# Kernel tuning notes

Hardware: AMD Instinct MI355X
Metric: run time of the kernel (lower is better)

The kernel has to match this reference:

```python
import jax, jax.numpy as jnp
import numpy as np

B, S, D, DEPTH = 2, 2048, 1024, 4
NUM_LEAVES = 2 ** DEPTH          # 16
NUM_DEC = NUM_LEAVES - 1         # 15


def setup_inputs() -> dict:
    key = jax.random.key(0)
    k1, k2, k3, k4, k5 = jax.random.split(key, 5)
    scale = 1.0 / np.sqrt(D)
    return {
        "x": jax.random.normal(k1, (B, S, D), dtype=jnp.float32),
        "dec_w": jax.random.normal(k2, (NUM_DEC, D), dtype=jnp.float32) * scale,
        "dec_b": jax.random.normal(k3, (NUM_DEC,), dtype=jnp.float32) * scale,
        "leaf_w": jax.random.normal(k4, (NUM_LEAVES, D, D), dtype=jnp.float32) * scale,  # [leaf, out, in] (torch Linear layout)
        "leaf_b": jax.random.normal(k5, (NUM_LEAVES, D), dtype=jnp.float32) * scale,
    }


def reference(x, dec_w, dec_b, leaf_w, leaf_b):
    num_leaves = leaf_w.shape[0]
    num_dec = num_leaves - 1
    # All decision-node sigmoids in one batched GEMM: [B,S,num_dec]
    dec = jax.nn.sigmoid(jnp.einsum("bsd,nd->bsn", x, dec_w) + dec_b)
    # Faithful to the original: each tree slot is multiplied exactly once by its
    # direct parent's decision (left child: p, right child: 1-p).
    leaf_idx = np.arange(num_dec, 2 * num_leaves - 1)      # slots holding leaf probs
    parent = (leaf_idx - 1) // 2                           # [num_leaves]
    is_left = (leaf_idx % 2 == 1)                          # [num_leaves]
    dec_p = dec[..., parent]                               # [B,S,num_leaves]
    leaf_probs = jnp.where(jnp.asarray(is_left), dec_p, 1.0 - dec_p)
    # All leaf MLPs as one batched GEMM: [B,S,L,D]
    leaf_out = jnp.einsum("bsd,lod->bslo", x, leaf_w) + leaf_b
    # Probability-weighted sum over leaves -> [B,S,D]
    return jnp.einsum("bslo,bsl->bso", leaf_out, leaf_probs)
```

## Files before the change

kernel.cpp:

```cpp
#include <hip/hip_runtime.h>
#include <stdint.h>


#define M_TOK 4096
#define DDIM  1024
#define KFLAT 9216

typedef __bf16 bf16x8 __attribute__((ext_vector_type(8)));
typedef float  f32x4  __attribute__((ext_vector_type(4)));
typedef unsigned short u16x4 __attribute__((ext_vector_type(4)));
typedef unsigned short u16x8 __attribute__((ext_vector_type(8)));

#define GLB(p) ((const __attribute__((address_space(1))) void*)(p))
#define LDS(p) ((__attribute__((address_space(3))) void*)(p))

__device__ __forceinline__ unsigned short f2bf(float f) {
    union { float f; uint32_t u; } v; v.f = f;
    uint32_t u = v.u;
    return (unsigned short)((u + 0x7fffu + ((u >> 16) & 1u)) >> 16);
}

__global__ __launch_bounds__(256) void prep_dec_kernel(
    const float* __restrict__ x, const float* __restrict__ dec_w,
    const float* __restrict__ dec_b, const float* __restrict__ lw,
    const float* __restrict__ lb, unsigned short* __restrict__ wp,
    float* __restrict__ bw, unsigned short* __restrict__ xs,
    float* __restrict__ pmat)
{
    if (blockIdx.x < 1024) {
        int idx = blockIdx.x * 256 + threadIdx.x;
        int o  = idx >> 8;
        int k4 = (idx & 255) << 2;
        size_t src = (size_t)o * DDIM + k4;
        size_t dstb = (size_t)o * KFLAT + k4;
        float4 acc = make_float4(0.f, 0.f, 0.f, 0.f);
#pragma unroll
        for (int j = 0; j < 8; ++j) {
            const float4 a = *(const float4*)(lw + (size_t)(2*j)   * DDIM*DDIM + src);
            const float4 b = *(const float4*)(lw + (size_t)(2*j+1) * DDIM*DDIM + src);
            u16x4 d;
            d[0] = f2bf(a.x - b.x); d[1] = f2bf(a.y - b.y);
            d[2] = f2bf(a.z - b.z); d[3] = f2bf(a.w - b.w);
            *(u16x4*)(wp + dstb + (size_t)j * DDIM) = d;
            acc.x += b.x; acc.y += b.y; acc.z += b.z; acc.w += b.w;
        }
        u16x4 s;
        s[0] = f2bf(acc.x); s[1] = f2bf(acc.y); s[2] = f2bf(acc.z); s[3] = f2bf(acc.w);
        *(u16x4*)(wp + dstb + (size_t)8 * DDIM) = s;
        if ((idx & 255) == 0) {
            float sb = 0.f;
#pragma unroll
            for (int j = 0; j < 8; ++j) {
                float ba = lb[(2*j) * DDIM + o];
                float bb = lb[(2*j+1) * DDIM + o];
                bw[j * DDIM + o] = ba - bb;
                sb += bb;
            }
            bw[8 * DDIM + o] = sb;
        }
    } else {
        int m    = (blockIdx.x - 1024) * 4 + (threadIdx.x >> 6);
        int lane = threadIdx.x & 63;
        const float* xr = x + (size_t)m * DDIM + lane * 16;
        float xv[16];
        *(float4*)&xv[0]  = *(const float4*)(xr + 0);
        *(float4*)&xv[4]  = *(const float4*)(xr + 4);
        *(float4*)&xv[8]  = *(const float4*)(xr + 8);
        *(float4*)&xv[12] = *(const float4*)(xr + 12);
        float s[8];
#pragma unroll
        for (int j = 0; j < 8; ++j) {
            const float* wr = dec_w + (size_t)(7 + j) * DDIM + lane * 16;
            float a = 0.f;
#pragma unroll
            for (int i = 0; i < 16; i += 4) {
                float4 wv = *(const float4*)(wr + i);
                a = fmaf(xv[i], wv.x, fmaf(xv[i+1], wv.y, fmaf(xv[i+2], wv.z, fmaf(xv[i+3], wv.w, a))));
            }
            s[j] = a;
        }
#pragma unroll
        for (int j = 0; j < 8; ++j)
#pragma unroll
            for (int off = 32; off > 0; off >>= 1)
                s[j] += __shfl_xor(s[j], off);
        float p[8];
#pragma unroll
        for (int j = 0; j < 8; ++j)
            p[j] = 1.0f / (1.0f + expf(-(s[j] + dec_b[7 + j])));
        if (lane == 0) {
#pragma unroll
            for (int j = 0; j < 8; ++j)
                pmat[(size_t)m * 8 + j] = p[j];
        }
#pragma unroll
        for (int j = 0; j < 9; ++j) {
            float pj = (j < 8) ? p[j] : 1.0f;
            unsigned short* dst = xs + (size_t)m * KFLAT + j * DDIM + lane * 16;
#pragma unroll
            for (int c = 0; c < 2; ++c) {
                u16x8 o;
#pragma unroll
                for (int e = 0; e < 8; ++e) o[e] = f2bf(pj * xv[c * 8 + e]);
                *(u16x8*)(dst + c * 8) = o;
            }
        }
    }
}

__global__ __launch_bounds__(256, 4) void tree_gemm3(
    const unsigned short* __restrict__ xs,
    const unsigned short* __restrict__ wp,
    const float* __restrict__ bw,
    const float* __restrict__ pmat,
    float* __restrict__ out,
    float* __restrict__ parts,
    int KG)
{
    __shared__ __align__(16) unsigned short Asm[2][128 * 32];
    __shared__ __align__(16) unsigned short Bsm[2][128 * 32];

    const int tid  = threadIdx.x;
    const int lane = tid & 63;
    const int w    = tid >> 6;
    const int wm   = w >> 1, wn = w & 1;
    const int bx   = blockIdx.x;
    const int xcd  = bx & 7;
    const int ii   = bx >> 3;
    const int mt   = xcd * 4 + (ii >> 3);
    const int nt   = ii & 7;
    const int m0   = mt * 128, n0 = nt * 128;
    const int g    = blockIdx.y;
    const int k0   = g * KG;
    const int ra   = lane & 15;
    const int kb   = (lane >> 4) * 8;

    f32x4 acc[4][4] = {};

    auto stage = [&](int buf, int t) {
#pragma unroll
        for (int c = 0; c < 2; ++c) {
            int row = w * 32 + c * 16 + (lane >> 2);
            int ke  = k0 + t * 32 + (lane & 3) * 8;
            const unsigned short* ga = xs + (size_t)(m0 + row) * KFLAT + ke;
            __builtin_amdgcn_global_load_lds(GLB(ga), LDS(&Asm[buf][w * 1024 + c * 512]), 16, 0, 0);
            const unsigned short* gb = wp + (size_t)(n0 + row) * KFLAT + ke;
            __builtin_amdgcn_global_load_lds(GLB(gb), LDS(&Bsm[buf][w * 1024 + c * 512]), 16, 0, 0);
        }
    };

    const int TOT = KG >> 5;
    stage(0, 0);
    __syncthreads();
    int cur = 0;
    for (int t = 0; t < TOT; ++t) {
        if (t + 1 < TOT) stage(cur ^ 1, t + 1);

        bf16x8 av[4], bv[4];
#pragma unroll
        for (int i = 0; i < 4; ++i)
            av[i] = *(const bf16x8*)&Asm[cur][(wm * 64 + i * 16 + ra) * 32 + kb];
#pragma unroll
        for (int j = 0; j < 4; ++j)
            bv[j] = *(const bf16x8*)&Bsm[cur][(wn * 64 + j * 16 + ra) * 32 + kb];
#pragma unroll
        for (int i = 0; i < 4; ++i)
#pragma unroll
            for (int j = 0; j < 4; ++j)
                acc[i][j] = __builtin_amdgcn_mfma_f32_16x16x32_bf16(av[i], bv[j], acc[i][j], 0, 0, 0);

        __syncthreads();
        cur ^= 1;
    }

    float* bsm = (float*)&Asm[0][0];
    if (g == 0) {
        for (int idx = tid; idx < 9 * 128; idx += 256)
            bsm[idx] = bw[(idx >> 7) * DDIM + n0 + (idx & 127)];
    }
    __syncthreads();

    float* dst = (g == 0) ? out : parts + (size_t)(g - 1) * M_TOK * DDIM;
#pragma unroll
    for (int i = 0; i < 4; ++i)
#pragma unroll
        for (int r = 0; r < 4; ++r) {
            int row = m0 + wm * 64 + i * 16 + (lane >> 4) * 4 + r;
            float4 pa, pb;
            if (g == 0) {
                pa = *(const float4*)(pmat + (size_t)row * 8);
                pb = *(const float4*)(pmat + (size_t)row * 8 + 4);
            }
#pragma unroll
            for (int j = 0; j < 4; ++j) {
                int cl = wn * 64 + j * 16 + ra;
                float v = acc[i][j][r];
                if (g == 0) {
                    v += pa.x * bsm[0 * 128 + cl] + pa.y * bsm[1 * 128 + cl]
                       + pa.z * bsm[2 * 128 + cl] + pa.w * bsm[3 * 128 + cl]
                       + pb.x * bsm[4 * 128 + cl] + pb.y * bsm[5 * 128 + cl]
                       + pb.z * bsm[6 * 128 + cl] + pb.w * bsm[7 * 128 + cl]
                       + bsm[8 * 128 + cl];
                }
                dst[(size_t)row * DDIM + n0 + cl] = v;
            }
        }
}

__global__ __launch_bounds__(256) void reduce_kernel(
    float* __restrict__ out, const float* __restrict__ parts, int np)
{
    size_t i = (size_t)blockIdx.x * 256 + threadIdx.x;
    float4 a = ((const float4*)out)[i];
    for (int p = 0; p < np; ++p) {
        float4 b = ((const float4*)(parts + (size_t)p * M_TOK * DDIM))[i];
        a.x += b.x; a.y += b.y; a.z += b.z; a.w += b.w;
    }
    ((float4*)out)[i] = a;
}

extern "C" void kernel_launch(void* const* d_in, const int* in_sizes, int n_in,
                              void* d_out, int out_size, void* d_ws, size_t ws_size,
                              hipStream_t stream) {
    (void)in_sizes; (void)n_in; (void)out_size;
    const float* x     = (const float*)d_in[0];
    const float* dec_w = (const float*)d_in[1];
    const float* dec_b = (const float*)d_in[2];
    const float* lw    = (const float*)d_in[3];
    const float* lb    = (const float*)d_in[4];
    float* out = (float*)d_out;
    uint8_t* w8 = (uint8_t*)d_ws;

    unsigned short* xs   = (unsigned short*)(w8);
    unsigned short* wp   = (unsigned short*)(w8 + 75497472);
    float*          bw   = (float*)(w8 + 94371840);
    float*          pmat = (float*)(w8 + 94408704);
    float*          parts= (float*)(w8 + 94539776);
    const size_t NEED3 = 94539776 + 2ull * 16777216;
    const size_t NEED4 = 94539776 + 3ull * 16777216;

    int ks = (ws_size >= NEED4) ? 4 : (ws_size >= NEED3) ? 3 : 0;
    if (!ks) return;

    prep_dec_kernel<<<2048, 256, 0, stream>>>(x, dec_w, dec_b, lw, lb, wp, bw, xs, pmat);
    tree_gemm3<<<dim3(256, ks), 256, 0, stream>>>(xs, wp, bw, pmat, out, parts, KFLAT / ks);
    reduce_kernel<<<4096, 256, 0, stream>>>(out, parts, ks - 1);
}
```

Measured before the change: 149.9 us.

## Replace GEMM with 256x256-tile 8-wave kernel, swizzled LDS and bias folded into reduce

Adds a new GEMM kernel with 256x256 output tiles, 512 threads and 128KB of dynamic LDS. It uses a swizzled LDS layout, inline ds_read_b128, a hand-scheduled double-buffered pipeline with explicit vmcnt waits and barriers, and setprio around the MFMA groups. The probability-weighted bias epilogue moves out of the GEMM into a new reduce kernel. The aim is more data reuse per tile and better overlap of loads with MFMAs. The risk is fewer blocks (64 x ks), which may underfill the 256 CUs, and more barrier overhead.

```diff
diff --git a/kernel.cpp b/kernel.cpp
--- a/kernel.cpp
+++ b/kernel.cpp
@@ -18,6 +18,17 @@
     union { float f; uint32_t u; } v; v.f = f;
     uint32_t u = v.u;
     return (unsigned short)((u + 0x7fffu + ((u >> 16) & 1u)) >> 16);
+}
+
+__device__ __forceinline__ bf16x8 asbf(f32x4 v) {
+    bf16x8 r; __builtin_memcpy(&r, &v, 16); return r;
+}
+
+template<int OFF>
+__device__ __forceinline__ f32x4 dsr(uint32_t a) {
+    f32x4 r;
+    asm volatile("ds_read_b128 %0, %1 offset:%c2" : "=v"(r) : "v"(a), "i"(OFF));
+    return r;
 }
 
 __global__ __launch_bounds__(256) void prep_dec_kernel(
@@ -108,18 +119,178 @@
     }
 }
 
-__global__ __launch_bounds__(256, 4) void tree_gemm3(
+
+#define WAITV4 asm volatile("s_waitcnt vmcnt(4)" ::: "memory")
+#define WAITV0 asm volatile("s_waitcnt vmcnt(0)" ::: "memory")
+#define BARR   __builtin_amdgcn_s_barrier()
+#define LGKM0  do { asm volatile("s_waitcnt lgkmcnt(0)" ::: "memory"); \
+                    __builtin_amdgcn_sched_barrier(0); } while(0)
+
+#define READ_AV(q, b) do { \
+    av[0][0] = dsr<(b)*32768 + (2*(q)+0)*2048>(baseA0); \
+    av[0][1] = dsr<(b)*32768 + (2*(q)+0)*2048>(baseA1); \
+    av[1][0] = dsr<(b)*32768 + (2*(q)+1)*2048>(baseA0); \
+    av[1][1] = dsr<(b)*32768 + (2*(q)+1)*2048>(baseA1); \
+} while(0)
+
+#define READ_BV(b) do { \
+    bv[0][0] = dsr<(b)*32768 + 0*2048>(baseB0); bv[0][1] = dsr<(b)*32768 + 0*2048>(baseB1); \
+    bv[1][0] = dsr<(b)*32768 + 1*2048>(baseB0); bv[1][1] = dsr<(b)*32768 + 1*2048>(baseB1); \
+    bv[2][0] = dsr<(b)*32768 + 2*2048>(baseB0); bv[2][1] = dsr<(b)*32768 + 2*2048>(baseB1); \
+    bv[3][0] = dsr<(b)*32768 + 3*2048>(baseB0); bv[3][1] = dsr<(b)*32768 + 3*2048>(baseB1); \
+} while(0)
+
+#define MFMA_Q(q) do { \
+    __builtin_amdgcn_s_setprio(1); \
+    _Pragma("unroll") \
+    for (int mfl = 0; mfl < 2; ++mfl) { \
+        _Pragma("unroll") \
+        for (int j = 0; j < 4; ++j) { \
+            acc[2*(q)+mfl][j] = __builtin_amdgcn_mfma_f32_16x16x32_bf16(asbf(av[mfl][0]), asbf(bv[j][0]), acc[2*(q)+mfl][j], 0, 0, 0); \
+            acc[2*(q)+mfl][j] = __builtin_amdgcn_mfma_f32_16x16x32_bf16(asbf(av[mfl][1]), asbf(bv[j][1]), acc[2*(q)+mfl][j], 0, 0, 0); \
+        } \
+    } \
+    __builtin_amdgcn_s_setprio(0); \
+} while(0)
+
+__global__ __launch_bounds__(512, 2) void tree_gemm4(
     const unsigned short* __restrict__ xs,
     const unsigned short* __restrict__ wp,
-    const float* __restrict__ bw,
-    const float* __restrict__ pmat,
     float* __restrict__ out,
     float* __restrict__ parts,
     int KG)
 {
+    extern __shared__ char smem[];
+    const int tid  = threadIdx.x;
+    const int lane = tid & 63;
+    const int w    = tid >> 6;
+    const int wm   = w >> 2, wn = w & 3;
+    const int ra   = lane & 15;
+    const int g16  = lane >> 4;
+
+    const int bx  = blockIdx.x;
+    const int xcd = bx & 7, ii = bx >> 3;
+    const int nt  = xcd >> 1;
+    const int mt  = (xcd & 1) * 8 + ii;
+    const int m0  = mt * 256, n0 = nt * 256;
+    const int g   = blockIdx.y;
+    const int k0  = g * KG;
+    const int NI  = KG >> 7;
+
+    uint32_t sbase = (uint32_t)(uintptr_t)(__attribute__((address_space(3))) char*)smem;
+
+    const uint32_t colb0 = (uint32_t)(((ra & 1) << 6) | (((g16 + ((ra >> 1) & 3)) & 3) << 4));
+    const uint32_t colb1 = colb0 ^ 64;
+    const uint32_t baseA0 = sbase + wm * 16384 + ra * 128 + colb0;
+    const uint32_t baseA1 = sbase + wm * 16384 + ra * 128 + colb1;
+    const uint32_t baseB0 = sbase + 65536 + wn * 8192 + ra * 128 + colb0;
+    const uint32_t baseB1 = sbase + 65536 + wn * 8192 + ra * 128 + colb1;
+
+    const int sh  = ((lane >> 2) ^ (lane >> 3)) & 1;
+    const int sc  = ((lane & 3) - ((lane >> 4) & 3)) & 3;
+    const int kel = sh * 32 + sc * 8;
+    const int rA  = w * 8 + (lane >> 3);
+
+    auto stageA = [&](int buf, int tt, int hh) {
+        const unsigned short* s0 = xs + (size_t)(m0 + hh * 128 + rA) * KFLAT + (k0 + tt * 64 + kel);
+        char* d0 = smem + buf * 32768 + hh * 16384 + w * 1024;
+        __builtin_amdgcn_global_load_lds(GLB(s0), LDS(d0), 16, 0, 0);
+        __builtin_amdgcn_global_load_lds(GLB(s0 + (size_t)64 * KFLAT), LDS(d0 + 8192), 16, 0, 0);
+    };
+    auto stageB = [&](int buf, int tt, int hh) {
+        const unsigned short* s0 = wp + (size_t)(n0 + hh * 128 + rA) * KFLAT + (k0 + tt * 64 + kel);
+        char* d0 = smem + 65536 + buf * 32768 + hh * 16384 + w * 1024;
+        __builtin_amdgcn_global_load_lds(GLB(s0), LDS(d0), 16, 0, 0);
+        __builtin_amdgcn_global_load_lds(GLB(s0 + (size_t)64 * KFLAT), LDS(d0 + 8192), 16, 0, 0);
+    };
+
+    f32x4 acc[8][4] = {};
+    f32x4 av[2][2], bv[4][2];
+
+    stageA(0, 0, 0); stageA(0, 0, 1);
+    stageB(0, 0, 0); stageB(0, 0, 1);
+    stageB(1, 1, 0); stageB(1, 1, 1);
+    WAITV4;
+    BARR;
+
+    for (int i = 0; i < NI; ++i) {
+        const int t = 2 * i;
+        const bool on = (i + 1 < NI);
+
+        READ_BV(0); READ_AV(0, 0);
+        stageA(1, t + 1, 0); stageA(1, t + 1, 1);
+        BARR; LGKM0; MFMA_Q(0); BARR;
+        READ_AV(1, 0);
+        if (on) stageB(0, t + 2, 0);
+        BARR; LGKM0; MFMA_Q(1); BARR;
+        READ_AV(2, 0);
+        if (on) stageB(0, t + 2, 1);
+        BARR; LGKM0; MFMA_Q(2); BARR;
+        READ_AV(3, 0);
+        BARR; LGKM0; MFMA_Q(3);
+        if (on) { WAITV4; } else { WAITV0; }
+        BARR;
+
+        READ_BV(1); READ_AV(0, 1);
+        if (on) { stageA(0, t + 2, 0); stageA(0, t + 2, 1); }
+        BARR; LGKM0; MFMA_Q(0); BARR;
+        READ_AV(1, 1);
+        if (on) stageB(1, t + 3, 0);
+        BARR; LGKM0; MFMA_Q(1); BARR;
+        READ_AV(2, 1);
+        if (on) stageB(1, t + 3, 1);
+        BARR; LGKM0; MFMA_Q(2); BARR;
+        READ_AV(3, 1);
+        BARR; LGKM0; MFMA_Q(3);
+        if (on) WAITV4;
+        BARR;
+    }
+
+    float* dst = (g == 0) ? out : parts + (size_t)(g - 1) * M_TOK * DDIM;
+#pragma unroll
+    for (int mf = 0; mf < 8; ++mf)
+#pragma unroll
+        for (int e = 0; e < 4; ++e) {
+            int row = m0 + wm * 128 + mf * 16 + g16 * 4 + e;
+#pragma unroll
+            for (int j = 0; j < 4; ++j)
+                dst[(size_t)row * DDIM + n0 + wn * 64 + j * 16 + ra] = acc[mf][j][e];
+        }
+}
+
+__global__ __launch_bounds__(256) void reduce2_kernel(
+    float* __restrict__ out, const float* __restrict__ parts,
+    const float* __restrict__ pmat, const float* __restrict__ bw, int np)
+{
+    size_t i = (size_t)blockIdx.x * 256 + threadIdx.x;
+    int m   = (int)(i >> 8);
+    int col = (int)(i & 255) * 4;
+    float4 a = ((const float4*)out)[i];
+    for (int p = 0; p < np; ++p) {
+        float4 b = ((const float4*)(parts + (size_t)p * M_TOK * DDIM))[i];
+        a.x += b.x; a.y += b.y; a.z += b.z; a.w += b.w;
+    }
+    float4 pa = *(const float4*)(pmat + (size_t)m * 8);
+    float4 pb = *(const float4*)(pmat + (size_t)m * 8 + 4);
+    float4 bias = *(const float4*)(bw + 8 * DDIM + col);
+#pragma unroll
+    for (int l = 0; l < 8; ++l) {
+        float pl = (l < 4) ? ((const float*)&pa)[l] : ((const float*)&pb)[l - 4];
+        float4 bl = *(const float4*)(bw + l * DDIM + col);
+        bias.x = fmaf(pl, bl.x, bias.x); bias.y = fmaf(pl, bl.y, bias.y);
+        bias.z = fmaf(pl, bl.z, bias.z); bias.w = fmaf(pl, bl.w, bias.w);
+    }
+    a.x += bias.x; a.y += bias.y; a.z += bias.z; a.w += bias.w;
+    ((float4*)out)[i] = a;
+}
+
+__global__ __launch_bounds__(256, 4) void tree_gemm3(
+    const unsigned short* __restrict__ xs, const unsigned short* __restrict__ wp,
+    const float* __restrict__ bw, const float* __restrict__ pmat,
+    float* __restrict__ out, float* __restrict__ parts, int KG)
+{
     __shared__ __align__(16) unsigned short Asm[2][128 * 32];
     __shared__ __align__(16) unsigned short Bsm[2][128 * 32];
-
     const int tid  = threadIdx.x;
     const int lane = tid & 63;
     const int w    = tid >> 6;
@@ -134,9 +305,7 @@
     const int k0   = g * KG;
     const int ra   = lane & 15;
     const int kb   = (lane >> 4) * 8;
-
     f32x4 acc[4][4] = {};
-
     auto stage = [&](int buf, int t) {
 #pragma unroll
         for (int c = 0; c < 2; ++c) {
@@ -148,44 +317,39 @@
             __builtin_amdgcn_global_load_lds(GLB(gb), LDS(&Bsm[buf][w * 1024 + c * 512]), 16, 0, 0);
         }
     };
-
     const int TOT = KG >> 5;
     stage(0, 0);
     __syncthreads();
     int cur = 0;
     for (int t = 0; t < TOT; ++t) {
         if (t + 1 < TOT) stage(cur ^ 1, t + 1);
-
-        bf16x8 av[4], bv[4];
-#pragma unroll
-        for (int i = 0; i < 4; ++i)
-            av[i] = *(const bf16x8*)&Asm[cur][(wm * 64 + i * 16 + ra) * 32 + kb];
+        bf16x8 av2[4], bv2[4];
+#pragma unroll
+        for (int i2 = 0; i2 < 4; ++i2)
+            av2[i2] = *(const bf16x8*)&Asm[cur][(wm * 64 + i2 * 16 + ra) * 32 + kb];
 #pragma unroll
         for (int j = 0; j < 4; ++j)
-            bv[j] = *(const bf16x8*)&Bsm[cur][(wn * 64 + j * 16 + ra) * 32 + kb];
-#pragma unroll
-        for (int i = 0; i < 4; ++i)
+            bv2[j] = *(const bf16x8*)&Bsm[cur][(wn * 64 + j * 16 + ra) * 32 + kb];
+#pragma unroll
+        for (int i2 = 0; i2 < 4; ++i2)
 #pragma unroll
             for (int j = 0; j < 4; ++j)
-                acc[i][j] = __builtin_amdgcn_mfma_f32_16x16x32_bf16(av[i], bv[j], acc[i][j], 0, 0, 0);
-
+                acc[i2][j] = __builtin_amdgcn_mfma_f32_16x16x32_bf16(av2[i2], bv2[j], acc[i2][j], 0, 0, 0);
         __syncthreads();
         cur ^= 1;
     }
-
     float* bsm = (float*)&Asm[0][0];
     if (g == 0) {
         for (int idx = tid; idx < 9 * 128; idx += 256)
             bsm[idx] = bw[(idx >> 7) * DDIM + n0 + (idx & 127)];
     }
     __syncthreads();
-
     float* dst = (g == 0) ? out : parts + (size_t)(g - 1) * M_TOK * DDIM;
 #pragma unroll
-    for (int i = 0; i < 4; ++i)
+    for (int i2 = 0; i2 < 4; ++i2)
 #pragma unroll
         for (int r = 0; r < 4; ++r) {
-            int row = m0 + wm * 64 + i * 16 + (lane >> 4) * 4 + r;
+            int row = m0 + wm * 64 + i2 * 16 + (lane >> 4) * 4 + r;
             float4 pa, pb;
             if (g == 0) {
                 pa = *(const float4*)(pmat + (size_t)row * 8);
@@ -194,7 +358,7 @@
 #pragma unroll
             for (int j = 0; j < 4; ++j) {
                 int cl = wn * 64 + j * 16 + ra;
-                float v = acc[i][j][r];
+                float v = acc[i2][j][r];
                 if (g == 0) {
                     v += pa.x * bsm[0 * 128 + cl] + pa.y * bsm[1 * 128 + cl]
                        + pa.z * bsm[2 * 128 + cl] + pa.w * bsm[3 * 128 + cl]
@@ -243,6 +407,15 @@
     if (!ks) return;
 
     prep_dec_kernel<<<2048, 256, 0, stream>>>(x, dec_w, dec_b, lw, lb, wp, bw, xs, pmat);
-    tree_gemm3<<<dim3(256, ks), 256, 0, stream>>>(xs, wp, bw, pmat, out, parts, KFLAT / ks);
-    reduce_kernel<<<4096, 256, 0, stream>>>(out, parts, ks - 1);
-}
+
+    hipError_t e = hipFuncSetAttribute(
+        reinterpret_cast<const void*>(tree_gemm4),
+        hipFuncAttributeMaxDynamicSharedMemorySize, 131072);
+    if (e == hipSuccess) {
+        tree_gemm4<<<dim3(64, ks), 512, 131072, stream>>>(xs, wp, out, parts, KFLAT / ks);
+        reduce2_kernel<<<4096, 256, 0, stream>>>(out, parts, pmat, bw, ks - 1);
+    } else {
+        tree_gemm3<<<dim3(256, ks), 256, 0, stream>>>(xs, wp, bw, pmat, out, parts, KFLAT / ks);
+        reduce_kernel<<<4096, 256, 0, stream>>>(out, parts, ks - 1);
+    }
+}
```

Measured after the change: 130.0 us. 13.3% less time.
